# Performance work log

Measured on AMD Instinct MI355X. Metric: run time of the kernel, lower is better.

## Reference

```python
import jax, jax.numpy as jnp
import numpy as np


def setup_inputs() -> dict:
    key = jax.random.key(0)
    k1, k2, k3, k4 = jax.random.split(key, 4)
    B, S, IN, H = 4, 2048, 512, 1024
    x = jax.random.normal(k1, (B, S, IN), dtype=jnp.float32)
    W1 = jax.random.normal(k2, (IN, H), dtype=jnp.float32) * (1.0 / np.sqrt(IN))
    b1 = jax.random.normal(k3, (H,), dtype=jnp.float32) * 0.02
    Wq = jax.random.normal(k4, (H, H), dtype=jnp.float32) * (1.0 / np.sqrt(H))
    return {"x": x, "W1": W1, "b1": b1, "Wq": Wq, "atten_size": 16}


def reference(x, W1, b1, Wq, atten_size):
    A = atten_size
    B, S, _ = x.shape
    H = W1.shape[1]
    h = jax.nn.relu(jnp.einsum('bsi,ih->bsh', x, W1) + b1)  # [B,S,H]
    # zero-pad sequence dim by A on each side
    padded = jnp.pad(h, ((0, 0), (A, A), (0, 0)))  # [B,S+2A,H]
    # torch: stack(roll(padded, k, 1) for k in -A..A, dim=2) then slice [A:-A]
    # => x_nei[b, i, j] = padded[b, 2A + i - j]
    idx = 2 * A + jnp.arange(S)[:, None] - jnp.arange(2 * A + 1)[None, :]  # [S,W]
    x_nei = padded[:, idx, :]  # [B,S,W,H]
    q = jnp.einsum('bsh,hk->bsk', h, Wq)  # [B,S,H]
    scores = jnp.einsum('bsh,bswh->bsw', q, x_nei) / jnp.sqrt(jnp.asarray(H, x.dtype))
    w = jax.nn.softmax(scores, axis=2)  # softmax over window axis
    out = jnp.einsum('bsw,bswh->bsh', w, x_nei)
    return out
```

## Files before the change

kernel.cpp:

```cpp
#include <hip/hip_runtime.h>
#include <stdint.h>

constexpr int BATCH = 4;
constexpr int SEQ   = 2048;
constexpr int DIN   = 512;
constexpr int DH    = 1024;
constexpr int BS    = BATCH * SEQ;
constexpr int AP    = 32;
constexpr int AW    = 64;

typedef float  floatx4 __attribute__((ext_vector_type(4)));
typedef short  bf16x8  __attribute__((ext_vector_type(8)));

static __device__ __forceinline__ unsigned short f2bf(float f) {
  union { float f; unsigned u; } v; v.f = f;
  unsigned r = (v.u + 0x7fffu + ((v.u >> 16) & 1u)) >> 16;
  return (unsigned short)r;
}

static __device__ __forceinline__ void gld_lds16(const unsigned short* g, const short* l) {
  typedef const __attribute__((address_space(1))) void* gvp;
  typedef __attribute__((address_space(3))) void* lvp;
  __builtin_amdgcn_global_load_lds((gvp)(uintptr_t)g, (lvp)(unsigned)(uintptr_t)l, 16, 0, 0);
}

__global__ __launch_bounds__(256) void transpose_w_k(const float* __restrict__ W1,
                                                     const float* __restrict__ Wq,
                                                     unsigned short* __restrict__ w1t,
                                                     unsigned short* __restrict__ wqt) {
  __shared__ float t[32][33];
  const bool isW1 = blockIdx.y < 16;
  const float* in = isW1 ? W1 : Wq;
  unsigned short* out = isW1 ? w1t : wqt;
  const int R = isW1 ? DIN : DH;
  const int C = DH;
  const int r0 = (isW1 ? blockIdx.y : (blockIdx.y - 16)) * 32;
  const int c0 = blockIdx.x * 32;
  const int tx = threadIdx.x & 31, ty = threadIdx.x >> 5;
  for (int i = ty; i < 32; i += 8) t[i][tx] = in[(size_t)(r0 + i) * C + c0 + tx];
  __syncthreads();
  for (int i = ty; i < 32; i += 8) out[(size_t)(c0 + i) * R + r0 + tx] = f2bf(t[tx][i]);
}

__global__ __launch_bounds__(256) void gemm1_k(const float* __restrict__ X,
                                               const unsigned short* __restrict__ Bt,
                                               const float* __restrict__ bias,
                                               unsigned short* __restrict__ outB,
                                               unsigned short* __restrict__ outBT) {
  const int M = BS, N = DH, K = DIN;
  __shared__ __align__(16) short As0[128 * 32], As1[128 * 32];
  __shared__ __align__(16) short Bs0[128 * 32], Bs1[128 * 32];
  const int tid  = threadIdx.x;
  const int m0   = blockIdx.x * 128, n0 = blockIdx.y * 128;
  const int wv   = tid >> 6, lane = tid & 63;
  const int wm   = (wv >> 1) * 64, wn = (wv & 1) * 64;
  const int l16  = lane & 15, quad = lane >> 4;

  const int ar = tid >> 1, acol = (tid & 1) * 16;
  const float* gX = X + (size_t)(m0 + ar) * K + acol;
  short* lA0 = &As0[ar * 32 + acol];
  short* lA1 = &As1[ar * 32 + acol];
  const int ra = lane >> 2, ca = (lane & 3) * 8;
  const unsigned short* gB = Bt + (size_t)(n0 + wv * 32 + ra) * K + ca;
  const short* lB0a = &Bs0[wv * 1024];
  const short* lB0b = &Bs0[wv * 1024 + 512];
  const short* lB1a = &Bs1[wv * 1024];
  const short* lB1b = &Bs1[wv * 1024 + 512];

  floatx4 acc[4][4];
  for (int i = 0; i < 4; i++)
    for (int j = 0; j < 4; j++) acc[i][j] = {0.f, 0.f, 0.f, 0.f};

  for (int ks = 0; ks < K / 64; ++ks) {
    float4 x0 = ((const float4*)gX)[0], x1 = ((const float4*)gX)[1];
    float4 x2 = ((const float4*)gX)[2], x3 = ((const float4*)gX)[3];
    float4 x4 = ((const float4*)(gX + 32))[0], x5 = ((const float4*)(gX + 32))[1];
    float4 x6 = ((const float4*)(gX + 32))[2], x7 = ((const float4*)(gX + 32))[3];
    gX += 64;
    __align__(16) unsigned short c0[16], c1[16];
    c0[0] = f2bf(x0.x); c0[1] = f2bf(x0.y); c0[2]  = f2bf(x0.z); c0[3]  = f2bf(x0.w);
    c0[4] = f2bf(x1.x); c0[5] = f2bf(x1.y); c0[6]  = f2bf(x1.z); c0[7]  = f2bf(x1.w);
    c0[8] = f2bf(x2.x); c0[9] = f2bf(x2.y); c0[10] = f2bf(x2.z); c0[11] = f2bf(x2.w);
    c0[12] = f2bf(x3.x); c0[13] = f2bf(x3.y); c0[14] = f2bf(x3.z); c0[15] = f2bf(x3.w);
    c1[0] = f2bf(x4.x); c1[1] = f2bf(x4.y); c1[2]  = f2bf(x4.z); c1[3]  = f2bf(x4.w);
    c1[4] = f2bf(x5.x); c1[5] = f2bf(x5.y); c1[6]  = f2bf(x5.z); c1[7]  = f2bf(x5.w);
    c1[8] = f2bf(x6.x); c1[9] = f2bf(x6.y); c1[10] = f2bf(x6.z); c1[11] = f2bf(x6.w);
    c1[12] = f2bf(x7.x); c1[13] = f2bf(x7.y); c1[14] = f2bf(x7.z); c1[15] = f2bf(x7.w);
    __syncthreads();
    gld_lds16(gB, lB0a); gld_lds16(gB + 16 * K, lB0b);
    gld_lds16(gB + 32, lB1a); gld_lds16(gB + 16 * K + 32, lB1b);
    gB += 64;
    ((uint4*)lA0)[0] = ((uint4*)c0)[0];
    ((uint4*)lA0)[1] = ((uint4*)c0)[1];
    ((uint4*)lA1)[0] = ((uint4*)c1)[0];
    ((uint4*)lA1)[1] = ((uint4*)c1)[1];
    __syncthreads();
    bf16x8 af[4], bfr[4];
    for (int i = 0; i < 4; i++)
      af[i] = *(const bf16x8*)&As0[(wm + i * 16 + l16) * 32 + quad * 8];
    for (int j = 0; j < 4; j++)
      bfr[j] = *(const bf16x8*)&Bs0[(wn + j * 16 + l16) * 32 + quad * 8];
    for (int i = 0; i < 4; i++)
      for (int j = 0; j < 4; j++)
        acc[i][j] = __builtin_amdgcn_mfma_f32_16x16x32_bf16(af[i], bfr[j], acc[i][j], 0, 0, 0);
    for (int i = 0; i < 4; i++)
      af[i] = *(const bf16x8*)&As1[(wm + i * 16 + l16) * 32 + quad * 8];
    for (int j = 0; j < 4; j++)
      bfr[j] = *(const bf16x8*)&Bs1[(wn + j * 16 + l16) * 32 + quad * 8];
    for (int i = 0; i < 4; i++)
      for (int j = 0; j < 4; j++)
        acc[i][j] = __builtin_amdgcn_mfma_f32_16x16x32_bf16(af[i], bfr[j], acc[i][j], 0, 0, 0);
  }

  for (int j = 0; j < 4; j++) {
    const int col = n0 + wn + j * 16 + l16;
    const float bv = bias[col];
    for (int i = 0; i < 4; i++) {
      const int rowb = m0 + wm + i * 16 + quad * 4;
      float v[4];
      for (int r = 0; r < 4; r++) v[r] = fmaxf(acc[i][j][r] + bv, 0.f);
      for (int r = 0; r < 4; r++) outB[(size_t)(rowb + r) * N + col] = f2bf(v[r]);
      ushort4 o4; o4.x = f2bf(v[0]); o4.y = f2bf(v[1]); o4.z = f2bf(v[2]); o4.w = f2bf(v[3]);
      *(ushort4*)(outBT + (size_t)col * M + rowb) = o4;
    }
  }
}

__global__ __launch_bounds__(256) void gemm2_k(const unsigned short* __restrict__ Ab,
                                               const unsigned short* __restrict__ Bt,
                                               unsigned short* __restrict__ outB) {
  const int N = DH, K = DH;
  __shared__ __align__(16) short As0[128 * 32], As1[128 * 32];
  __shared__ __align__(16) short Bs0[128 * 32], Bs1[128 * 32];
  const int tid  = threadIdx.x;
  const int m0   = blockIdx.x * 128, n0 = blockIdx.y * 128;
  const int wv   = tid >> 6, lane = tid & 63;
  const int wm   = (wv >> 1) * 64, wn = (wv & 1) * 64;
  const int l16  = lane & 15, quad = lane >> 4;

  const int ra = lane >> 2, ca = (lane & 3) * 8;
  const unsigned short* gA = Ab + (size_t)(m0 + wv * 32 + ra) * K + ca;
  const unsigned short* gB = Bt + (size_t)(n0 + wv * 32 + ra) * K + ca;
  const short* lA0a = &As0[wv * 1024];
  const short* lA0b = &As0[wv * 1024 + 512];
  const short* lA1a = &As1[wv * 1024];
  const short* lA1b = &As1[wv * 1024 + 512];
  const short* lB0a = &Bs0[wv * 1024];
  const short* lB0b = &Bs0[wv * 1024 + 512];
  const short* lB1a = &Bs1[wv * 1024];
  const short* lB1b = &Bs1[wv * 1024 + 512];

  floatx4 acc[4][4];
  for (int i = 0; i < 4; i++)
    for (int j = 0; j < 4; j++) acc[i][j] = {0.f, 0.f, 0.f, 0.f};

  for (int ks = 0; ks < K / 64; ++ks) {
    __syncthreads();
    gld_lds16(gA, lA0a); gld_lds16(gA + 16 * K, lA0b);
    gld_lds16(gA + 32, lA1a); gld_lds16(gA + 16 * K + 32, lA1b);
    gld_lds16(gB, lB0a); gld_lds16(gB + 16 * K, lB0b);
    gld_lds16(gB + 32, lB1a); gld_lds16(gB + 16 * K + 32, lB1b);
    gA += 64; gB += 64;
    __syncthreads();
    bf16x8 af[4], bfr[4];
    for (int i = 0; i < 4; i++)
      af[i] = *(const bf16x8*)&As0[(wm + i * 16 + l16) * 32 + quad * 8];
    for (int j = 0; j < 4; j++)
      bfr[j] = *(const bf16x8*)&Bs0[(wn + j * 16 + l16) * 32 + quad * 8];
    for (int i = 0; i < 4; i++)
      for (int j = 0; j < 4; j++)
        acc[i][j] = __builtin_amdgcn_mfma_f32_16x16x32_bf16(af[i], bfr[j], acc[i][j], 0, 0, 0);
    for (int i = 0; i < 4; i++)
      af[i] = *(const bf16x8*)&As1[(wm + i * 16 + l16) * 32 + quad * 8];
    for (int j = 0; j < 4; j++)
      bfr[j] = *(const bf16x8*)&Bs1[(wn + j * 16 + l16) * 32 + quad * 8];
    for (int i = 0; i < 4; i++)
      for (int j = 0; j < 4; j++)
        acc[i][j] = __builtin_amdgcn_mfma_f32_16x16x32_bf16(af[i], bfr[j], acc[i][j], 0, 0, 0);
  }

  for (int j = 0; j < 4; j++) {
    const int col = n0 + wn + j * 16 + l16;
    for (int i = 0; i < 4; i++) {
      const int rowb = m0 + wm + i * 16 + quad * 4;
      for (int r = 0; r < 4; r++)
        outB[(size_t)(rowb + r) * N + col] = f2bf(acc[i][j][r]);
    }
  }
}

__global__ __launch_bounds__(512) void attn_mfma_k(const unsigned short* __restrict__ hb,
                                                   const unsigned short* __restrict__ hbT,
                                                   const unsigned short* __restrict__ qb,
                                                   float* __restrict__ out) {
  __shared__ float Sf[32 * 64];
  __shared__ __align__(16) short Ps[32 * 72];

  const int tid  = threadIdx.x;
  const int wave = tid >> 6, lane = tid & 63;
  const int l16  = lane & 15, quad = lane >> 4;
  const int p0   = blockIdx.x * AP;
  const int s0   = p0 & (SEQ - 1);

  for (int i = tid; i < 32 * 72 / 2; i += 512) ((unsigned*)Ps)[i] = 0;

  {
    const int mt = wave >> 2, nt = wave & 3;
    const unsigned short* qp = qb + (size_t)(p0 + mt * 16 + l16) * DH + quad * 8;
    const int hrow = s0 - 16 + nt * 16 + l16;
    const bool hv = (hrow >= 0) && (hrow < SEQ);
    const unsigned short* hp = hb + (long long)(p0 - 16 + nt * 16 + l16) * DH + quad * 8;

    floatx4 ac[4] = {{0,0,0,0},{0,0,0,0},{0,0,0,0},{0,0,0,0}};
    const bf16x8 hz = {0,0,0,0,0,0,0,0};
    #pragma unroll
    for (int it = 0; it < 32; ++it) {
      bf16x8 qa = *(const bf16x8*)(qp + it * 32);
      bf16x8 ha = hz;
      if (hv) ha = *(const bf16x8*)(hp + it * 32);
      ac[it & 3] = __builtin_amdgcn_mfma_f32_16x16x32_bf16(qa, ha, ac[it & 3], 0, 0, 0);
    }
    floatx4 s4;
    for (int r = 0; r < 4; r++)
      s4[r] = (ac[0][r] + ac[1][r]) + (ac[2][r] + ac[3][r]);
    for (int r = 0; r < 4; r++)
      Sf[(mt * 16 + quad * 4 + r) * 64 + nt * 16 + l16] = s4[r] * (1.f / 32.f);
  }
  __syncthreads();

  {
    const int row = tid >> 4, k = tid & 15;
    const float v0 = Sf[row * 64 + row + k];
    const float v1 = Sf[row * 64 + row + k + 16];
    const float v2 = (k == 0) ? Sf[row * 64 + row + 32] : -1e30f;
    float mx = fmaxf(v0, fmaxf(v1, v2));
    for (int off = 1; off < 16; off <<= 1) mx = fmaxf(mx, __shfl_xor(mx, off, 64));
    const float e0 = __expf(v0 - mx), e1 = __expf(v1 - mx);
    const float e2 = (k == 0) ? __expf(v2 - mx) : 0.f;
    float sum = e0 + e1 + e2;
    for (int off = 1; off < 16; off <<= 1) sum += __shfl_xor(sum, off, 64);
    const float inv = 1.f / sum;
    Ps[row * 72 + row + k] = f2bf(e0 * inv);
    Ps[row * 72 + row + k + 16] = f2bf(e1 * inv);
    if (k == 0) Ps[row * 72 + row + 32] = f2bf(e2 * inv);
  }
  __syncthreads();

  {
    const bf16x8 pb00 = *(const bf16x8*)&Ps[(l16) * 72 + quad * 8];
    const bf16x8 pb01 = *(const bf16x8*)&Ps[(l16) * 72 + 32 + quad * 8];
    const bf16x8 pb10 = *(const bf16x8*)&Ps[(16 + l16) * 72 + quad * 8];
    const bf16x8 pb11 = *(const bf16x8*)&Ps[(16 + l16) * 72 + 32 + quad * 8];

    int lo = 16 - s0; if (lo < 0) lo = 0;
    int hi = SEQ + 16 - s0; if (hi > AW) hi = AW;
    const bool interior = (lo == 0) && (hi == AW);

    #pragma unroll
    for (int i = 0; i < 8; ++i) {
      const int mt2 = wave * 8 + i;
      const unsigned short* ap = hbT + (size_t)(mt2 * 16 + l16) * BS + (p0 - 16) + quad * 8;
      bf16x8 aa0 = *(const bf16x8*)(ap);
      bf16x8 aa1 = *(const bf16x8*)(ap + 32);
      if (!interior) {
        #pragma unroll
        for (int j = 0; j < 8; j++) {
          const int k = quad * 8 + j;
          if (k < lo || k >= hi) aa0[j] = 0;
          if (k + 32 < lo || k + 32 >= hi) aa1[j] = 0;
        }
      }
      floatx4 o0 = {0.f, 0.f, 0.f, 0.f}, o1 = {0.f, 0.f, 0.f, 0.f};
      o0 = __builtin_amdgcn_mfma_f32_16x16x32_bf16(aa0, pb00, o0, 0, 0, 0);
      o0 = __builtin_amdgcn_mfma_f32_16x16x32_bf16(aa1, pb01, o0, 0, 0, 0);
      o1 = __builtin_amdgcn_mfma_f32_16x16x32_bf16(aa0, pb10, o1, 0, 0, 0);
      o1 = __builtin_amdgcn_mfma_f32_16x16x32_bf16(aa1, pb11, o1, 0, 0, 0);
      float4 s0v; s0v.x = o0[0]; s0v.y = o0[1]; s0v.z = o0[2]; s0v.w = o0[3];
      float4 s1v; s1v.x = o1[0]; s1v.y = o1[1]; s1v.z = o1[2]; s1v.w = o1[3];
      *(float4*)(out + (size_t)(p0 + l16) * DH + mt2 * 16 + quad * 4) = s0v;
      *(float4*)(out + (size_t)(p0 + 16 + l16) * DH + mt2 * 16 + quad * 4) = s1v;
    }
  }
}

extern "C" void kernel_launch(void* const* d_in, const int* in_sizes, int n_in,
                              void* d_out, int out_size, void* d_ws, size_t ws_size,
                              hipStream_t stream) {
  const float* x  = (const float*)d_in[0];
  const float* W1 = (const float*)d_in[1];
  const float* b1 = (const float*)d_in[2];
  const float* Wq = (const float*)d_in[3];

  char* w = (char*)d_ws;
  unsigned short* w1t = (unsigned short*)(w);
  unsigned short* wqt = (unsigned short*)(w + (1ull  << 20));
  unsigned short* hb  = (unsigned short*)(w + (3ull  << 20));
  unsigned short* hbT = (unsigned short*)(w + (19ull << 20));
  unsigned short* qb  = (unsigned short*)(w + (35ull << 20));

  transpose_w_k<<<dim3(DH / 32, 48), 256, 0, stream>>>(W1, Wq, w1t, wqt);

  gemm1_k<<<dim3(BS / 128, DH / 128), 256, 0, stream>>>(x, w1t, b1, hb, hbT);
  gemm2_k<<<dim3(BS / 128, DH / 128), 256, 0, stream>>>(hb, wqt, qb);

  attn_mfma_k<<<BS / AP, 512, 0, stream>>>(hb, hbT, qb, (float*)d_out);
}
```

Before: 157.3 us.

## Pre-convert x to bf16 and load A tiles via direct-to-LDS copies

Adds a separate kernel that converts x to bf16 once, writing into the q buffer's workspace slot. gemm1 then stages A tiles with global_load_lds, just as it already does for B, instead of doing fp32 loads, in-register conversion and LDS stores. The goal is to avoid redoing the conversion for each of the 8 N-tiles and to shorten the load path. The cost is an extra launch plus a bf16 round trip through memory. It also adds s_setprio around the MFMA sections of the attention kernel to favour waves issuing matrix ops.

```diff
diff --git a/kernel.cpp b/kernel.cpp
--- a/kernel.cpp
+++ b/kernel.cpp
@@ -22,6 +22,17 @@
   typedef const __attribute__((address_space(1))) void* gvp;
   typedef __attribute__((address_space(3))) void* lvp;
   __builtin_amdgcn_global_load_lds((gvp)(uintptr_t)g, (lvp)(unsigned)(uintptr_t)l, 16, 0, 0);
+}
+
+__global__ __launch_bounds__(256) void convert_x_k(const float* __restrict__ X,
+                                                   unsigned short* __restrict__ Xb) {
+  const int t = blockIdx.x * 256 + threadIdx.x;
+  const float4 a = ((const float4*)X)[(size_t)t * 2];
+  const float4 b = ((const float4*)X)[(size_t)t * 2 + 1];
+  __align__(16) unsigned short o[8];
+  o[0] = f2bf(a.x); o[1] = f2bf(a.y); o[2] = f2bf(a.z); o[3] = f2bf(a.w);
+  o[4] = f2bf(b.x); o[5] = f2bf(b.y); o[6] = f2bf(b.z); o[7] = f2bf(b.w);
+  *(uint4*)(Xb + (size_t)t * 8) = *(const uint4*)o;
 }
 
 __global__ __launch_bounds__(256) void transpose_w_k(const float* __restrict__ W1,
@@ -42,7 +53,7 @@
   for (int i = ty; i < 32; i += 8) out[(size_t)(c0 + i) * R + r0 + tx] = f2bf(t[tx][i]);
 }
 
-__global__ __launch_bounds__(256) void gemm1_k(const float* __restrict__ X,
+__global__ __launch_bounds__(256) void gemm1_k(const unsigned short* __restrict__ Ab,
                                                const unsigned short* __restrict__ Bt,
                                                const float* __restrict__ bias,
                                                unsigned short* __restrict__ outB,
@@ -56,12 +67,13 @@
   const int wm   = (wv >> 1) * 64, wn = (wv & 1) * 64;
   const int l16  = lane & 15, quad = lane >> 4;
 
-  const int ar = tid >> 1, acol = (tid & 1) * 16;
-  const float* gX = X + (size_t)(m0 + ar) * K + acol;
-  short* lA0 = &As0[ar * 32 + acol];
-  short* lA1 = &As1[ar * 32 + acol];
   const int ra = lane >> 2, ca = (lane & 3) * 8;
+  const unsigned short* gA = Ab + (size_t)(m0 + wv * 32 + ra) * K + ca;
   const unsigned short* gB = Bt + (size_t)(n0 + wv * 32 + ra) * K + ca;
+  const short* lA0a = &As0[wv * 1024];
+  const short* lA0b = &As0[wv * 1024 + 512];
+  const short* lA1a = &As1[wv * 1024];
+  const short* lA1b = &As1[wv * 1024 + 512];
   const short* lB0a = &Bs0[wv * 1024];
   const short* lB0b = &Bs0[wv * 1024 + 512];
   const short* lB1a = &Bs1[wv * 1024];
@@ -72,28 +84,12 @@
     for (int j = 0; j < 4; j++) acc[i][j] = {0.f, 0.f, 0.f, 0.f};
 
   for (int ks = 0; ks < K / 64; ++ks) {
-    float4 x0 = ((const float4*)gX)[0], x1 = ((const float4*)gX)[1];
-    float4 x2 = ((const float4*)gX)[2], x3 = ((const float4*)gX)[3];
-    float4 x4 = ((const float4*)(gX + 32))[0], x5 = ((const float4*)(gX + 32))[1];
-    float4 x6 = ((const float4*)(gX + 32))[2], x7 = ((const float4*)(gX + 32))[3];
-    gX += 64;
-    __align__(16) unsigned short c0[16], c1[16];
-    c0[0] = f2bf(x0.x); c0[1] = f2bf(x0.y); c0[2]  = f2bf(x0.z); c0[3]  = f2bf(x0.w);
-    c0[4] = f2bf(x1.x); c0[5] = f2bf(x1.y); c0[6]  = f2bf(x1.z); c0[7]  = f2bf(x1.w);
-    c0[8] = f2bf(x2.x); c0[9] = f2bf(x2.y); c0[10] = f2bf(x2.z); c0[11] = f2bf(x2.w);
-    c0[12] = f2bf(x3.x); c0[13] = f2bf(x3.y); c0[14] = f2bf(x3.z); c0[15] = f2bf(x3.w);
-    c1[0] = f2bf(x4.x); c1[1] = f2bf(x4.y); c1[2]  = f2bf(x4.z); c1[3]  = f2bf(x4.w);
-    c1[4] = f2bf(x5.x); c1[5] = f2bf(x5.y); c1[6]  = f2bf(x5.z); c1[7]  = f2bf(x5.w);
-    c1[8] = f2bf(x6.x); c1[9] = f2bf(x6.y); c1[10] = f2bf(x6.z); c1[11] = f2bf(x6.w);
-    c1[12] = f2bf(x7.x); c1[13] = f2bf(x7.y); c1[14] = f2bf(x7.z); c1[15] = f2bf(x7.w);
     __syncthreads();
+    gld_lds16(gA, lA0a); gld_lds16(gA + 16 * K, lA0b);
+    gld_lds16(gA + 32, lA1a); gld_lds16(gA + 16 * K + 32, lA1b);
     gld_lds16(gB, lB0a); gld_lds16(gB + 16 * K, lB0b);
     gld_lds16(gB + 32, lB1a); gld_lds16(gB + 16 * K + 32, lB1b);
-    gB += 64;
-    ((uint4*)lA0)[0] = ((uint4*)c0)[0];
-    ((uint4*)lA0)[1] = ((uint4*)c0)[1];
-    ((uint4*)lA1)[0] = ((uint4*)c1)[0];
-    ((uint4*)lA1)[1] = ((uint4*)c1)[1];
+    gA += 64; gB += 64;
     __syncthreads();
     bf16x8 af[4], bfr[4];
     for (int i = 0; i < 4; i++)
@@ -213,6 +209,7 @@
 
     floatx4 ac[4] = {{0,0,0,0},{0,0,0,0},{0,0,0,0},{0,0,0,0}};
     const bf16x8 hz = {0,0,0,0,0,0,0,0};
+    __builtin_amdgcn_s_setprio(1);
     #pragma unroll
     for (int it = 0; it < 32; ++it) {
       bf16x8 qa = *(const bf16x8*)(qp + it * 32);
@@ -220,6 +217,7 @@
       if (hv) ha = *(const bf16x8*)(hp + it * 32);
       ac[it & 3] = __builtin_amdgcn_mfma_f32_16x16x32_bf16(qa, ha, ac[it & 3], 0, 0, 0);
     }
+    __builtin_amdgcn_s_setprio(0);
     floatx4 s4;
     for (int r = 0; r < 4; r++)
       s4[r] = (ac[0][r] + ac[1][r]) + (ac[2][r] + ac[3][r]);
@@ -271,10 +269,12 @@
         }
       }
       floatx4 o0 = {0.f, 0.f, 0.f, 0.f}, o1 = {0.f, 0.f, 0.f, 0.f};
+      __builtin_amdgcn_s_setprio(1);
       o0 = __builtin_amdgcn_mfma_f32_16x16x32_bf16(aa0, pb00, o0, 0, 0, 0);
       o0 = __builtin_amdgcn_mfma_f32_16x16x32_bf16(aa1, pb01, o0, 0, 0, 0);
       o1 = __builtin_amdgcn_mfma_f32_16x16x32_bf16(aa0, pb10, o1, 0, 0, 0);
       o1 = __builtin_amdgcn_mfma_f32_16x16x32_bf16(aa1, pb11, o1, 0, 0, 0);
+      __builtin_amdgcn_s_setprio(0);
       float4 s0v; s0v.x = o0[0]; s0v.y = o0[1]; s0v.z = o0[2]; s0v.w = o0[3];
       float4 s1v; s1v.x = o1[0]; s1v.y = o1[1]; s1v.z = o1[2]; s1v.w = o1[3];
       *(float4*)(out + (size_t)(p0 + l16) * DH + mt2 * 16 + quad * 4) = s0v;
@@ -297,10 +297,12 @@
   unsigned short* hb  = (unsigned short*)(w + (3ull  << 20));
   unsigned short* hbT = (unsigned short*)(w + (19ull << 20));
   unsigned short* qb  = (unsigned short*)(w + (35ull << 20));
-
+  unsigned short* xb  = qb;
+
+  convert_x_k<<<BS * DIN / (256 * 8), 256, 0, stream>>>(x, xb);
   transpose_w_k<<<dim3(DH / 32, 48), 256, 0, stream>>>(W1, Wq, w1t, wqt);
 
-  gemm1_k<<<dim3(BS / 128, DH / 128), 256, 0, stream>>>(x, w1t, b1, hb, hbT);
+  gemm1_k<<<dim3(BS / 128, DH / 128), 256, 0, stream>>>(xb, w1t, b1, hb, hbT);
   gemm2_k<<<dim3(BS / 128, DH / 128), 256, 0, stream>>>(hb, wqt, qb);
 
   attn_mfma_k<<<BS / AP, 512, 0, stream>>>(hb, hbT, qb, (float*)d_out);
```

Result: no change. 155.7 us (-1.0%).
